# Kernel optimization log

Measured on AMD Instinct MI355X. Metric: run time of the kernel, lower is better.

Reference implementation:

```python
import jax, jax.numpy as jnp
import numpy as np

N, E, G, B, L = 24576, 98304, 512, 512, 1000
F_IN, H1, C1, C2, HID = 5, 2, 64, 128, 256


def setup_inputs() -> dict:
    key = jax.random.key(0)
    ks = jax.random.split(key, 20)
    rn = lambda k, s: jax.random.normal(k, s, jnp.float32) * 0.1
    return {
        "x": jax.random.normal(ks[0], (N, F_IN), jnp.float32),
        "edge_index": jax.random.randint(ks[1], (2, E), 0, N),
        "batch": jnp.sort(jax.random.randint(ks[2], (N,), 0, G)),
        "protein_seq": jax.random.randint(ks[3], (B, L), 0, 22),
        "W1": rn(ks[4], (F_IN, H1 * C1)), "att_src1": rn(ks[5], (H1, C1)), "att_dst1": rn(ks[6], (H1, C1)), "b1": jnp.zeros((H1 * C1,), jnp.float32),
        "W2": rn(ks[7], (H1 * C1, C2)), "att_src2": rn(ks[8], (1, C2)), "att_dst2": rn(ks[9], (1, C2)), "b2": jnp.zeros((C2,), jnp.float32),
        "Wd": rn(ks[10], (C2, HID)), "bd": jnp.zeros((HID,), jnp.float32),
        "Pe": rn(ks[11], (22, 64)),
        "K1": rn(ks[12], (64, 64, 3)), "bk1": jnp.zeros((64,), jnp.float32),
        "K2": rn(ks[13], (128, 64, 5)), "bk2": jnp.zeros((128,), jnp.float32),
        "Wp": rn(ks[14], (128, HID)), "bp": jnp.zeros((HID,), jnp.float32),
        "Wf1": rn(ks[15], (2 * HID, 128)), "bf1": jnp.zeros((128,), jnp.float32),
        "Wf2": rn(ks[16], (128, 64)), "bf2": jnp.zeros((64,), jnp.float32),
        "Wo": rn(ks[17], (64, 1)), "bo": jnp.zeros((1,), jnp.float32),
    }


def _gat(x, edge_index, W, att_src, att_dst, b, heads, out_ch):
    """PyG GATConv: add self-loops, per-edge LeakyReLU(0.2) scores, segment softmax over dst."""
    n = x.shape[0]
    h = (x @ W).reshape(n, heads, out_ch)
    loop = jnp.arange(n)
    src = jnp.concatenate([edge_index[0], loop])
    dst = jnp.concatenate([edge_index[1], loop])
    a_s = jnp.sum(h * att_src[None], axis=-1)  # [n, H]
    a_d = jnp.sum(h * att_dst[None], axis=-1)
    e = jax.nn.leaky_relu(a_s[src] + a_d[dst], negative_slope=0.2)  # [E+n, H]
    m = jax.ops.segment_max(e, dst, num_segments=n)
    w = jnp.exp(e - m[dst])
    den = jax.ops.segment_sum(w, dst, num_segments=n)
    alpha = w / (den[dst] + 1e-16)
    out = jax.ops.segment_sum(h[src] * alpha[..., None], dst, num_segments=n)
    return out.reshape(n, heads * out_ch) + b


def _conv1d(x, k, pad):  # x: [B,C,L], k: [O,I,K]
    return jax.lax.conv_general_dilated(x, k, (1,), [(pad, pad)], dimension_numbers=("NCH", "OIH", "NCH"))


def reference(x, edge_index, batch, protein_seq, W1, att_src1, att_dst1, b1, W2, att_src2, att_dst2, b2, Wd, bd, Pe, K1, bk1, K2, bk2, Wp, bp, Wf1, bf1, Wf2, bf2, Wo, bo):
    # drug branch (GAT x2 + global mean pool)
    g = jax.nn.elu(_gat(x, edge_index, W1, att_src1, att_dst1, b1, H1, C1))
    g = jax.nn.elu(_gat(g, edge_index, W2, att_src2, att_dst2, b2, 1, C2))
    sums = jax.ops.segment_sum(g, batch, num_segments=G)
    cnt = jax.ops.segment_sum(jnp.ones((g.shape[0], 1), g.dtype), batch, num_segments=G)
    drug = jax.nn.relu(sums / jnp.maximum(cnt, 1.0) @ Wd + bd)
    # protein branch (embed -> conv1d x2 -> global max pool)
    pe = Pe[protein_seq].transpose(0, 2, 1)  # [B, 64, L]
    p = jax.nn.elu(_conv1d(pe, K1, 1) + bk1[None, :, None])
    p = jax.nn.elu(_conv1d(p, K2, 2) + bk2[None, :, None])
    prot = jax.nn.relu(jnp.max(p, axis=2) @ Wp + bp)
    # head
    h = jnp.concatenate([drug, prot], axis=1)
    h = jax.nn.relu(h @ Wf1 + bf1)
    h = jax.nn.relu(h @ Wf2 + bf2)
    return h @ Wo + bo
```

## Files before the change

kernel.cpp:

```cpp
#include <hip/hip_runtime.h>
#include <hip/hip_bf16.h>
#include <math.h>

#define NN 24576
#define NE 98304
#define ETOT (NE + NN)
#define NG 512
#define NB 512
#define LL 1000
#define TL 124
#define NTILE 9

typedef __attribute__((ext_vector_type(8))) short short8;
typedef __attribute__((ext_vector_type(4))) short short4v;
typedef __attribute__((ext_vector_type(4))) float f32x4;

__device__ inline short f2bf(float x) {
    union { __hip_bfloat16 b; short s; } u;
    u.b = __float2bfloat16(x);
    return u.s;
}

__device__ inline float bf2f(short s) {
    return __uint_as_float(((unsigned)(unsigned short)s) << 16);
}

__device__ inline void atomicMaxFloat(float* addr, float val) {
    int* ai = (int*)addr;
    int old = __float_as_int(*addr);
    while (__int_as_float(old) < val) {
        int assumed = old;
        old = atomicCAS(ai, assumed, __float_as_int(val));
        if (old == assumed) break;
    }
}

__global__ void k_init(int* deg, int* cursor, float* sums, float* cnt, float* pmax) {
    int i = blockIdx.x * 256 + threadIdx.x;
    if (i < NN) { deg[i] = 0; cursor[i] = 0; }
    if (i < NG * 128) sums[i] = 0.f;
    if (i < NG) cnt[i] = 0.f;
    if (i < NB * 128) pmax[i] = -1e30f;
}

__global__ void k_count(const int* ei, int* deg) {
    int e = blockIdx.x * 256 + threadIdx.x;
    if (e >= ETOT) return;
    int d = (e < NE) ? ei[NE + e] : e - NE;
    atomicAdd(&deg[d], 1);
}

__global__ void k_scan1(const int* deg, int* excl, int* part) {
    __shared__ int s[256];
    int b = blockIdx.x, t = threadIdx.x, i = b * 256 + t;
    int v = deg[i];
    s[t] = v;
    __syncthreads();
    for (int o = 1; o < 256; o <<= 1) {
        int x = (t >= o) ? s[t - o] : 0;
        __syncthreads();
        s[t] += x;
        __syncthreads();
    }
    excl[i] = s[t] - v;
    if (t == 255) part[b] = s[t];
}

__global__ void k_scan2(int* part) {
    __shared__ int s[96];
    int t = threadIdx.x;
    if (t < 96) s[t] = part[t];
    __syncthreads();
    if (t == 0) {
        int run = 0;
        for (int i = 0; i < 96; i++) { int v = s[i]; s[i] = run; run += v; }
    }
    __syncthreads();
    if (t < 96) part[t] = s[t];
}

__global__ void k_scan3(const int* excl, const int* part, int* rowptr) {
    int i = blockIdx.x * 256 + threadIdx.x;
    rowptr[i] = excl[i] + part[i >> 8];
    if (i == 0) rowptr[NN] = ETOT;
}

__global__ void k_scatter(const int* ei, const int* rowptr, int* cursor, int* colidx) {
    int e = blockIdx.x * 256 + threadIdx.x;
    if (e >= ETOT) return;
    int s, d;
    if (e < NE) { s = ei[e]; d = ei[NE + e]; }
    else { s = d = e - NE; }
    int pos = atomicAdd(&cursor[d], 1);
    colidx[rowptr[d] + pos] = s;
}

__global__ void k_as1(const float* x, const float* wvec, float* as_, float* ad_) {
    int idx = blockIdx.x * 256 + threadIdx.x;
    if (idx >= NN * 2) return;
    int n = idx >> 1, hd = idx & 1;
    float s = 0.f, dv = 0.f;
#pragma unroll
    for (int f = 0; f < 5; f++) {
        float xv = x[n * 5 + f];
        s += xv * wvec[hd * 5 + f];
        dv += xv * wvec[10 + hd * 5 + f];
    }
    as_[idx] = s;
    ad_[idx] = dv;
}

__global__ void k_agg2x(const int* rowptr, const int* colidx, const float* x,
                        const float* as_, const float* ad_,
                        const float* W1, const float* b1, const float* wvec,
                        unsigned int* g1b, float* as2, float* ad2) {
    __shared__ float sW[640];
    __shared__ float sb1[128];
    __shared__ float swa[256];
    int t = threadIdx.x;
    for (int i = t; i < 640; i += 256) sW[i] = W1[i];
    if (t < 128) { sb1[t] = b1[t]; swa[t] = wvec[32 + t]; swa[128 + t] = wvec[160 + t]; }
    __syncthreads();

    int d = blockIdx.x * 16 + (t >> 4);
    int g = t & 15;
    int hd = (g < 5) ? 0 : 1;
    int f = (g < 5) ? g : g - 5;
    float adv = ad_[d * 2 + hd];
    int p0 = rowptr[d], p1 = rowptr[d + 1];
    float m = -1e30f, den = 0.f, acc = 0.f;
    if (g < 10) {
        for (int pc = p0; pc < p1; pc += 4) {
            int sarr[4]; float ev[4], xv[4];
#pragma unroll
            for (int i = 0; i < 4; i++) {
                int pp = pc + i;
                sarr[i] = colidx[pp < p1 ? pp : p1 - 1];
            }
#pragma unroll
            for (int i = 0; i < 4; i++) {
                ev[i] = as_[sarr[i] * 2 + hd];
                xv[i] = x[sarr[i] * 5 + f];
            }
#pragma unroll
            for (int i = 0; i < 4; i++) {
                if (pc + i < p1) {
                    float e = ev[i] + adv;
                    e = e >= 0.f ? e : 0.2f * e;
                    float nm = fmaxf(m, e);
                    float sc = __expf(m - nm);
                    float w = __expf(e - nm);
                    den = den * sc + w;
                    acc = acc * sc + w * xv[i];
                    m = nm;
                }
            }
        }
    }
    float xn = acc / (den + 1e-16f);
    int gb = (t & 63) & ~15;
    int hcol = g >> 3;
    float xs[5];
#pragma unroll
    for (int f2 = 0; f2 < 5; f2++)
        xs[f2] = __shfl(xn, gb + hcol * 5 + f2, 64);
    float ps = 0.f, pd = 0.f;
    float g1v[8];
#pragma unroll
    for (int k = 0; k < 8; k++) {
        int col = g * 8 + k;
        float v = sb1[col];
#pragma unroll
        for (int f2 = 0; f2 < 5; f2++) v += xs[f2] * sW[f2 * 128 + col];
        v = v > 0.f ? v : __expf(v) - 1.f;
        g1v[k] = v;
        ps += v * swa[col];
        pd += v * swa[128 + col];
    }
    uint4 pk;
    pk.x = ((unsigned)(unsigned short)f2bf(g1v[1]) << 16) | (unsigned)(unsigned short)f2bf(g1v[0]);
    pk.y = ((unsigned)(unsigned short)f2bf(g1v[3]) << 16) | (unsigned)(unsigned short)f2bf(g1v[2]);
    pk.z = ((unsigned)(unsigned short)f2bf(g1v[5]) << 16) | (unsigned)(unsigned short)f2bf(g1v[4]);
    pk.w = ((unsigned)(unsigned short)f2bf(g1v[7]) << 16) | (unsigned)(unsigned short)f2bf(g1v[6]);
    *(uint4*)&g1b[d * 64 + g * 4] = pk;
#pragma unroll
    for (int msk = 1; msk < 16; msk <<= 1) {
        ps += __shfl_xor(ps, msk, 64);
        pd += __shfl_xor(pd, msk, 64);
    }
    if (g == 0) { as2[d] = ps; ad2[d] = pd; }
}

__global__ void k_agg1y(const int* rowptr, const int* colidx, const unsigned int* hb,
                        const float* as_, const float* ad_, float* yacc) {
    int t = threadIdx.x;
    int d = blockIdx.x * 4 + (t >> 6);
    int c = t & 63;
    float adv = ad_[d];
    int p0 = rowptr[d], p1 = rowptr[d + 1];
    float m = -1e30f, den = 0.f, acc0 = 0.f, acc1 = 0.f;
    for (int pc = p0; pc < p1; pc += 4) {
        int sarr[4]; float ev[4]; unsigned int hv[4];
#pragma unroll
        for (int i = 0; i < 4; i++) {
            int pp = pc + i;
            sarr[i] = colidx[pp < p1 ? pp : p1 - 1];
        }
#pragma unroll
        for (int i = 0; i < 4; i++) {
            ev[i] = as_[sarr[i]];
            hv[i] = hb[sarr[i] * 64 + c];
        }
#pragma unroll
        for (int i = 0; i < 4; i++) {
            if (pc + i < p1) {
                float e = ev[i] + adv;
                e = e >= 0.f ? e : 0.2f * e;
                float nm = fmaxf(m, e);
                float sc = __expf(m - nm);
                float w = __expf(e - nm);
                den = den * sc + w;
                float h0 = __uint_as_float(hv[i] << 16);
                float h1v = __uint_as_float(hv[i] & 0xFFFF0000u);
                acc0 = acc0 * sc + w * h0;
                acc1 = acc1 * sc + w * h1v;
                m = nm;
            }
        }
    }
    float inv = 1.f / (den + 1e-16f);
    ((float2*)yacc)[d * 64 + c] = (float2){acc0 * inv, acc1 * inv};
}

#define ASTR 136
__global__ __launch_bounds__(256, 2) void k_g2mm(
    const float* yacc, const short* Bh, const short* Bl, const float* b2, float* g2) {
    __shared__ __align__(16) short Ah[64 * ASTR];
    __shared__ __align__(16) short Al[64 * ASTR];
    int t = threadIdx.x;
    int m0 = blockIdx.x * 64;
    int wv = t >> 6, lane = t & 63;
    int ln15 = lane & 15, quad = lane >> 4;

    for (int i = t; i < 64 * 32; i += 256) {
        int row = i >> 5, c4 = (i & 31) * 4;
        float4 v = *(const float4*)&yacc[(m0 + row) * 128 + c4];
        short4v hi, lo;
        hi.x = f2bf(v.x); lo.x = f2bf(v.x - bf2f(hi.x));
        hi.y = f2bf(v.y); lo.y = f2bf(v.y - bf2f(hi.y));
        hi.z = f2bf(v.z); lo.z = f2bf(v.z - bf2f(hi.z));
        hi.w = f2bf(v.w); lo.w = f2bf(v.w - bf2f(hi.w));
        *(short4v*)&Ah[row * ASTR + c4] = hi;
        *(short4v*)&Al[row * ASTR + c4] = lo;
    }
    __syncthreads();

    f32x4 acc[8];
#pragma unroll
    for (int nt = 0; nt < 8; nt++) acc[nt] = (f32x4){0.f, 0.f, 0.f, 0.f};
    int arow = wv * 16 + ln15;
#pragma unroll
    for (int kb = 0; kb < 4; kb++) {
        int koff = kb * 32 + quad * 8;
        short8 a_hi = *(const short8*)&Ah[arow * ASTR + koff];
        short8 a_lo = *(const short8*)&Al[arow * ASTR + koff];
#pragma unroll
        for (int nt = 0; nt < 8; nt++) {
            short8 bh = *(const short8*)&Bh[((kb * 8 + nt) * 64 + lane) * 8];
            short8 bl = *(const short8*)&Bl[((kb * 8 + nt) * 64 + lane) * 8];
            acc[nt] = __builtin_amdgcn_mfma_f32_16x16x32_bf16(a_hi, bh, acc[nt], 0, 0, 0);
            acc[nt] = __builtin_amdgcn_mfma_f32_16x16x32_bf16(a_hi, bl, acc[nt], 0, 0, 0);
            acc[nt] = __builtin_amdgcn_mfma_f32_16x16x32_bf16(a_lo, bh, acc[nt], 0, 0, 0);
        }
    }
#pragma unroll
    for (int nt = 0; nt < 8; nt++) {
        int col = nt * 16 + ln15;
        float bias = b2[col];
#pragma unroll
        for (int r = 0; r < 4; r++) {
            float v = acc[nt][r] + bias;
            v = v > 0.f ? v : __expf(v) - 1.f;
            int n = m0 + wv * 16 + quad * 4 + r;
            g2[n * 128 + col] = v;
        }
    }
}

__global__ void k_pool(const float* g2, const int* batch, float* sums, float* cnt) {
    __shared__ int sb[96];
    int blk = blockIdx.x, j = threadIdx.x;
    int n0 = blk * 96;
    if (j < 96) sb[j] = batch[n0 + j];
    __syncthreads();
    float v[4];
#pragma unroll
    for (int i = 0; i < 4; i++) v[i] = g2[(n0 + i) * 128 + j];
    int cur = sb[0], runStart = 0;
    float acc = 0.f;
    for (int q0 = 0; q0 < 96; q0 += 4) {
        float nv[4] = {0.f, 0.f, 0.f, 0.f};
        if (q0 + 4 < 96) {
#pragma unroll
            for (int i = 0; i < 4; i++) nv[i] = g2[(n0 + q0 + 4 + i) * 128 + j];
        }
#pragma unroll
        for (int i = 0; i < 4; i++) {
            int q = q0 + i;
            int bb = sb[q];
            if (bb != cur) {
                atomicAdd(&sums[cur * 128 + j], acc);
                if (j == 0) atomicAdd(&cnt[cur], (float)(q - runStart));
                cur = bb; acc = 0.f; runStart = q;
            }
            acc += v[i];
        }
#pragma unroll
        for (int i = 0; i < 4; i++) v[i] = nv[i];
    }
    atomicAdd(&sums[cur * 128 + j], acc);
    if (j == 0) atomicAdd(&cnt[cur], (float)(96 - runStart));
}

__global__ void k_drug_fc(const float* sums, const float* cnt, const float* Wd, const float* bd,
                          float* drug) {
    int idx = blockIdx.x * 256 + threadIdx.x;
    if (idx >= NG * 256) return;
    int g = idx >> 8, o = idx & 255;
    float c = cnt[g]; c = c < 1.f ? 1.f : c;
    float inv = 1.f / c;
    float acc = bd[o];
#pragma unroll 8
    for (int i = 0; i < 128; i++) acc += sums[g * 128 + i] * inv * Wd[i * 256 + o];
    drug[idx] = acc > 0.f ? acc : 0.f;
}

__global__ void k_prep_w(const float* K1, const float* K2, const float* W2, const float* Pe,
                         const float* W1, const float* as1c, const float* ad1c,
                         const float* as2c, const float* ad2c,
                         short* Bswz1, short* Bswz2, short* Bh2, short* Bl2, short* Peb,
                         float* wvec) {
    int idx = blockIdx.x * 256 + threadIdx.x;
    if (idx < 22 * 64) Peb[idx] = f2bf(Pe[idx]);
    if (idx < 20) {
        int q = idx % 10, hd = q / 5, f = q % 5;
        const float* av = (idx < 10) ? as1c : ad1c;
        float s = 0.f;
        for (int c = 0; c < 64; c++) s += W1[f * 128 + hd * 64 + c] * av[hd * 64 + c];
        wvec[idx < 10 ? q : 10 + q] = s;
    }
    if (idx >= 32 && idx < 288) {
        int q = idx - 32;
        int kk = q & 127;
        const float* av = (q < 128) ? as2c : ad2c;
        float s = 0.f;
        for (int n2 = 0; n2 < 128; n2++) s += W2[kk * 128 + n2] * av[n2];
        wvec[idx] = s;
    }
    if (idx < 192 * 64) {
        int j = idx & 7, lane = (idx >> 3) & 63, rest = idx >> 9;
        int nt = rest & 3, kb = rest >> 2;
        int k = kb * 32 + ((lane >> 4) << 3) + j;
        int n = nt * 16 + (lane & 15);
        int kk = k >> 6, i = k & 63;
        Bswz1[idx] = f2bf(K1[n * 192 + i * 3 + kk]);
    }
    if (idx < 320 * 128) {
        int j = idx & 7, lane = (idx >> 3) & 63, rest = idx >> 9;
        int nt = rest & 7, kb = rest >> 3;
        int k = kb * 32 + ((lane >> 4) << 3) + j;
        int n = nt * 16 + (lane & 15);
        int kk = k / 64, i = k % 64;
        Bswz2[idx] = f2bf(K2[n * 320 + i * 5 + kk]);
    }
    if (idx < 128 * 128) {
        int j = idx & 7, lane = (idx >> 3) & 63, rest = idx >> 9;
        int nt = rest & 7, kb = rest >> 3;
        int k = kb * 32 + ((lane >> 4) << 3) + j;
        int n = nt * 16 + (lane & 15);
        float v = W2[k * 128 + n];
        short hh = f2bf(v);
        Bh2[idx] = hh;
        Bl2[idx] = f2bf(v - bf2f(hh));
    }
}

#define SSTR 72
__global__ __launch_bounds__(256, 4) void k_protein(
    const int* seq, const short* Peb, const short* Bswz1, const float* bk1,
    const short* Bswz2, const float* bk2, float* pmax) {
    __shared__ __align__(16) short sEmb[130 * SSTR];
    __shared__ __align__(16) short s1[132 * SSTR];

    int b = blockIdx.x / NTILE;
    int tile = blockIdx.x - b * NTILE;
    int t0 = tile * TL;
    int t = threadIdx.x;
    int wv = t >> 6, lane = t & 63;
    int ln15 = lane & 15, quad = lane >> 4;
    int mhalf = wv & 1, nhalf = wv >> 1;

    for (int j0 = 0; j0 < 130; j0 += 64) {
        int j = j0 + (t >> 2);
        if (j < 130) {
            int c0 = (t & 3) * 16;
            int l = t0 - 3 + j;
            int id = (l >= 0 && l < LL) ? seq[b * LL + l] : -1;
            short* dst = &sEmb[j * SSTR + c0];
            if (id >= 0) {
                const short8* src = (const short8*)&Peb[id * 64 + c0];
                *(short8*)dst = src[0];
                *(short8*)(dst + 8) = src[1];
            } else {
                *(short8*)dst = (short8){0, 0, 0, 0, 0, 0, 0, 0};
                *(short8*)(dst + 8) = (short8){0, 0, 0, 0, 0, 0, 0, 0};
            }
        }
    }
    s1[(128 + (t >> 6)) * SSTR + (t & 63)] = 0;
    __syncthreads();

    {
        f32x4 acc[4][2];
#pragma unroll
        for (int mi = 0; mi < 4; mi++)
#pragma unroll
            for (int ni = 0; ni < 2; ni++) acc[mi][ni] = (f32x4){0.f, 0.f, 0.f, 0.f};
#pragma unroll
        for (int kb = 0; kb < 6; kb++) {
            int koff = kb * 32 + quad * 8;
            int kk = koff >> 6, i0 = koff & 63;
            short8 b0 = *(const short8*)&Bswz1[((kb * 4 + nhalf * 2 + 0) * 64 + lane) * 8];
            short8 b1 = *(const short8*)&Bswz1[((kb * 4 + nhalf * 2 + 1) * 64 + lane) * 8];
#pragma unroll
            for (int mi = 0; mi < 4; mi++) {
                int arow = (mhalf * 4 + mi) * 16 + ln15 + kk;
                short8 a = *(const short8*)&sEmb[arow * SSTR + i0];
                acc[mi][0] = __builtin_amdgcn_mfma_f32_16x16x32_bf16(a, b0, acc[mi][0], 0, 0, 0);
                acc[mi][1] = __builtin_amdgcn_mfma_f32_16x16x32_bf16(a, b1, acc[mi][1], 0, 0, 0);
            }
        }
#pragma unroll
        for (int mi = 0; mi < 4; mi++) {
            int mt = mhalf * 4 + mi;
#pragma unroll
            for (int ni = 0; ni < 2; ni++) {
                int col = (nhalf * 2 + ni) * 16 + ln15;
                float bias = bk1[col];
#pragma unroll
                for (int r = 0; r < 4; r++) {
                    int q = mt * 16 + quad * 4 + r;
                    int l = t0 - 2 + q;
                    float v = acc[mi][ni][r] + bias;
                    v = v > 0.f ? v : __expf(v) - 1.f;
                    s1[q * SSTR + col] = (l >= 0 && l < LL) ? f2bf(v) : (short)0;
                }
            }
        }
    }
    __syncthreads();

    f32x4 acc2[4][4];
#pragma unroll
    for (int mi = 0; mi < 4; mi++)
#pragma unroll
        for (int ni = 0; ni < 4; ni++) acc2[mi][ni] = (f32x4){0.f, 0.f, 0.f, 0.f};
#pragma unroll 2
    for (int kb = 0; kb < 10; kb++) {
        int koff = kb * 32 + quad * 8;
        int kk = koff >> 6, i0 = koff & 63;
        short8 a[4], bb[4];
#pragma unroll
        for (int mi = 0; mi < 4; mi++) {
            int arow = (mhalf * 4 + mi) * 16 + ln15 + kk;
            a[mi] = *(const short8*)&s1[arow * SSTR + i0];
        }
#pragma unroll
        for (int ni = 0; ni < 4; ni++)
            bb[ni] = *(const short8*)&Bswz2[((kb * 8 + nhalf * 4 + ni) * 64 + lane) * 8];
#pragma unroll
        for (int mi = 0; mi < 4; mi++)
#pragma unroll
            for (int ni = 0; ni < 4; ni++)
                acc2[mi][ni] = __builtin_amdgcn_mfma_f32_16x16x32_bf16(a[mi], bb[ni], acc2[mi][ni], 0, 0, 0);
    }

#pragma unroll
    for (int ni = 0; ni < 4; ni++) {
        int col = (nhalf * 4 + ni) * 16 + ln15;
        float mx = -1e30f;
#pragma unroll
        for (int mi = 0; mi < 4; mi++) {
#pragma unroll
            for (int r = 0; r < 4; r++) {
                int p = (mhalf * 4 + mi) * 16 + quad * 4 + r;
                if (p < TL && t0 + p < LL) mx = fmaxf(mx, acc2[mi][ni][r]);
            }
        }
        mx = fmaxf(mx, __shfl_xor(mx, 16, 64));
        mx = fmaxf(mx, __shfl_xor(mx, 32, 64));
        if (quad == 0) {
            float v = mx + bk2[col];
            v = v > 0.f ? v : __expf(v) - 1.f;
            atomicMaxFloat(&pmax[b * 128 + col], v);
        }
    }
}

__global__ void k_prot_fc(const float* pmax, const float* Wp, const float* bp, float* prot) {
    int idx = blockIdx.x * 256 + threadIdx.x;
    if (idx >= NB * 256) return;
    int g = idx >> 8, o = idx & 255;
    float acc = bp[o];
#pragma unroll 8
    for (int i = 0; i < 128; i++) acc += pmax[g * 128 + i] * Wp[i * 256 + o];
    prot[idx] = acc > 0.f ? acc : 0.f;
}

__global__ void k_head(const float* drug, const float* prot, const float* Wf1, const float* bf1,
                       const float* Wf2, const float* bf2, const float* Wo, const float* bo,
                       float* out) {
    __shared__ float in[512];
    __shared__ float hh[128];
    __shared__ float h2s[64];
    int g = blockIdx.x, t = threadIdx.x;
    in[t] = drug[g * 256 + t];
    in[128 + t] = drug[g * 256 + 128 + t];
    in[256 + t] = prot[g * 256 + t];
    in[384 + t] = prot[g * 256 + 128 + t];
    __syncthreads();
    float acc = bf1[t];
#pragma unroll 8
    for (int c = 0; c < 512; c++) acc += in[c] * Wf1[c * 128 + t];
    hh[t] = acc > 0.f ? acc : 0.f;
    __syncthreads();
    if (t < 64) {
        float a2 = bf2[t];
#pragma unroll 8
        for (int c = 0; c < 128; c++) a2 += hh[c] * Wf2[c * 64 + t];
        h2s[t] = a2 > 0.f ? a2 : 0.f;
    }
    __syncthreads();
    if (t == 0) {
        float o = bo[0];
#pragma unroll 8
        for (int c = 0; c < 64; c++) o += h2s[c] * Wo[c];
        out[g] = o;
    }
}

extern "C" void kernel_launch(void* const* d_in, const int* in_sizes, int n_in,
                              void* d_out, int out_size, void* d_ws, size_t ws_size,
                              hipStream_t stream) {
    (void)in_sizes; (void)n_in; (void)out_size; (void)ws_size;
    const float* x   = (const float*)d_in[0];
    const int* ei    = (const int*)d_in[1];
    const int* batch = (const int*)d_in[2];
    const int* seq   = (const int*)d_in[3];
    const float* W1  = (const float*)d_in[4];
    const float* a_s1 = (const float*)d_in[5];
    const float* a_d1 = (const float*)d_in[6];
    const float* b1  = (const float*)d_in[7];
    const float* W2  = (const float*)d_in[8];
    const float* a_s2 = (const float*)d_in[9];
    const float* a_d2 = (const float*)d_in[10];
    const float* b2  = (const float*)d_in[11];
    const float* Wd  = (const float*)d_in[12];
    const float* bd  = (const float*)d_in[13];
    const float* Pe  = (const float*)d_in[14];
    const float* K1  = (const float*)d_in[15];
    const float* bk1 = (const float*)d_in[16];
    const float* K2  = (const float*)d_in[17];
    const float* bk2 = (const float*)d_in[18];
    const float* Wp  = (const float*)d_in[19];
    const float* bp  = (const float*)d_in[20];
    const float* Wf1 = (const float*)d_in[21];
    const float* bf1 = (const float*)d_in[22];
    const float* Wf2 = (const float*)d_in[23];
    const float* bf2 = (const float*)d_in[24];
    const float* Wo  = (const float*)d_in[25];
    const float* bo  = (const float*)d_in[26];
    float* out = (float*)d_out;

    float* w = (float*)d_ws;
    float* g1bf = w; w += NN * 64;
    float* yacc = w; w += NN * 128;
    float* g2   = w; w += NN * 128;
    float* as1  = w; w += NN * 2;
    float* ad1  = w; w += NN * 2;
    float* as2  = w; w += NN;
    float* ad2  = w; w += NN;
    float* sums = w; w += NG * 128;
    float* cnt  = w; w += NG;
    float* drug = w; w += NG * 256;
    float* prot = w; w += NB * 256;
    float* pmax = w; w += NB * 128;
    float* wvec = w; w += 512;
    short* Bswz1 = (short*)w; w += 192 * 64 / 2;
    short* Bswz2 = (short*)w; w += 320 * 128 / 2;
    short* Bh2  = (short*)w; w += 128 * 128 / 2;
    short* Bl2  = (short*)w; w += 128 * 128 / 2;
    short* Peb  = (short*)w; w += 22 * 64 / 2 + 8;
    int* deg    = (int*)w; w += NN;
    int* cursor = (int*)w; w += NN;
    int* excl   = (int*)w; w += NN;
    int* part   = (int*)w; w += 128;
    int* rowptr = (int*)w; w += NN + 8;
    int* colidx = (int*)w; w += ETOT;

    unsigned int* g1b = (unsigned int*)g1bf;

    hipLaunchKernelGGL(k_init, dim3(256), dim3(256), 0, stream, deg, cursor, sums, cnt, pmax);
    hipLaunchKernelGGL(k_prep_w, dim3(160), dim3(256), 0, stream,
                       K1, K2, W2, Pe, W1, a_s1, a_d1, a_s2, a_d2,
                       Bswz1, Bswz2, Bh2, Bl2, Peb, wvec);

    hipLaunchKernelGGL(k_count, dim3(ETOT / 256), dim3(256), 0, stream, ei, deg);
    hipLaunchKernelGGL(k_scan1, dim3(NN / 256), dim3(256), 0, stream, deg, excl, part);
    hipLaunchKernelGGL(k_scan2, dim3(1), dim3(128), 0, stream, part);
    hipLaunchKernelGGL(k_scan3, dim3(NN / 256), dim3(256), 0, stream, excl, part, rowptr);
    hipLaunchKernelGGL(k_scatter, dim3(ETOT / 256), dim3(256), 0, stream, ei, rowptr, cursor, colidx);

    hipLaunchKernelGGL(k_protein, dim3(NB * NTILE), dim3(256), 0, stream,
                       seq, Peb, Bswz1, bk1, Bswz2, bk2, pmax);
    hipLaunchKernelGGL(k_prot_fc, dim3(NB), dim3(256), 0, stream, pmax, Wp, bp, prot);

    hipLaunchKernelGGL(k_as1, dim3(NN * 2 / 256), dim3(256), 0, stream, x, wvec, as1, ad1);
    hipLaunchKernelGGL(k_agg2x, dim3(NN / 16), dim3(256), 0, stream,
                       rowptr, colidx, x, as1, ad1, W1, b1, wvec, g1b, as2, ad2);

    hipLaunchKernelGGL(k_agg1y, dim3(NN / 4), dim3(256), 0, stream,
                       rowptr, colidx, g1b, as2, ad2, yacc);
    hipLaunchKernelGGL(k_g2mm, dim3(NN / 64), dim3(256), 0, stream,
                       yacc, Bh2, Bl2, b2, g2);

    hipLaunchKernelGGL(k_pool, dim3(NN / 96), dim3(128), 0, stream, g2, batch, sums, cnt);
    hipLaunchKernelGGL(k_drug_fc, dim3(NG), dim3(256), 0, stream, sums, cnt, Wd, bd, drug);

    hipLaunchKernelGGL(k_head, dim3(NG), dim3(128), 0, stream,
                       drug, prot, Wf1, bf1, Wf2, bf2, Wo, bo, out);
}
```

Measured before the change: 322.2 us.

## Merge small kernels to cut launches and overlap edge counting with protein conv

Folds init and weight prep into one launch, and runs degree counting and first-layer attention scores as extra blocks of the protein conv kernel so they overlap with it. Scan stages 2 and 3 are merged, with each block recomputing its own prefix. The protein FC, drug FC and MLP head become a single tail kernel, which removes the intermediate drug and prot buffers. The aim is to cut launch overhead and idle gaps between small kernels. In exchange, the protein kernel's grid is mixed with lightweight blocks that share its launch bounds and LDS allocation.

```diff
diff --git a/kernel.cpp b/kernel.cpp
--- a/kernel.cpp
+++ b/kernel.cpp
@@ -10,6 +10,9 @@
 #define LL 1000
 #define TL 124
 #define NTILE 9
+#define PROT_BLKS (NB * NTILE)
+#define CNT_BLKS (ETOT / 256)
+#define AS1_BLKS (NN * 2 / 256)
 
 typedef __attribute__((ext_vector_type(8))) short short8;
 typedef __attribute__((ext_vector_type(4))) short short4v;
@@ -35,312 +38,22 @@
     }
 }
 
-__global__ void k_init(int* deg, int* cursor, float* sums, float* cnt, float* pmax) {
-    int i = blockIdx.x * 256 + threadIdx.x;
-    if (i < NN) { deg[i] = 0; cursor[i] = 0; }
-    if (i < NG * 128) sums[i] = 0.f;
-    if (i < NG) cnt[i] = 0.f;
-    if (i < NB * 128) pmax[i] = -1e30f;
-}
-
-__global__ void k_count(const int* ei, int* deg) {
-    int e = blockIdx.x * 256 + threadIdx.x;
-    if (e >= ETOT) return;
-    int d = (e < NE) ? ei[NE + e] : e - NE;
-    atomicAdd(&deg[d], 1);
-}
-
-__global__ void k_scan1(const int* deg, int* excl, int* part) {
-    __shared__ int s[256];
-    int b = blockIdx.x, t = threadIdx.x, i = b * 256 + t;
-    int v = deg[i];
-    s[t] = v;
-    __syncthreads();
-    for (int o = 1; o < 256; o <<= 1) {
-        int x = (t >= o) ? s[t - o] : 0;
-        __syncthreads();
-        s[t] += x;
-        __syncthreads();
-    }
-    excl[i] = s[t] - v;
-    if (t == 255) part[b] = s[t];
-}
-
-__global__ void k_scan2(int* part) {
-    __shared__ int s[96];
-    int t = threadIdx.x;
-    if (t < 96) s[t] = part[t];
-    __syncthreads();
-    if (t == 0) {
-        int run = 0;
-        for (int i = 0; i < 96; i++) { int v = s[i]; s[i] = run; run += v; }
-    }
-    __syncthreads();
-    if (t < 96) part[t] = s[t];
-}
-
-__global__ void k_scan3(const int* excl, const int* part, int* rowptr) {
-    int i = blockIdx.x * 256 + threadIdx.x;
-    rowptr[i] = excl[i] + part[i >> 8];
-    if (i == 0) rowptr[NN] = ETOT;
-}
-
-__global__ void k_scatter(const int* ei, const int* rowptr, int* cursor, int* colidx) {
-    int e = blockIdx.x * 256 + threadIdx.x;
-    if (e >= ETOT) return;
-    int s, d;
-    if (e < NE) { s = ei[e]; d = ei[NE + e]; }
-    else { s = d = e - NE; }
-    int pos = atomicAdd(&cursor[d], 1);
-    colidx[rowptr[d] + pos] = s;
-}
-
-__global__ void k_as1(const float* x, const float* wvec, float* as_, float* ad_) {
-    int idx = blockIdx.x * 256 + threadIdx.x;
-    if (idx >= NN * 2) return;
-    int n = idx >> 1, hd = idx & 1;
-    float s = 0.f, dv = 0.f;
-#pragma unroll
-    for (int f = 0; f < 5; f++) {
-        float xv = x[n * 5 + f];
-        s += xv * wvec[hd * 5 + f];
-        dv += xv * wvec[10 + hd * 5 + f];
-    }
-    as_[idx] = s;
-    ad_[idx] = dv;
-}
-
-__global__ void k_agg2x(const int* rowptr, const int* colidx, const float* x,
-                        const float* as_, const float* ad_,
-                        const float* W1, const float* b1, const float* wvec,
-                        unsigned int* g1b, float* as2, float* ad2) {
-    __shared__ float sW[640];
-    __shared__ float sb1[128];
-    __shared__ float swa[256];
-    int t = threadIdx.x;
-    for (int i = t; i < 640; i += 256) sW[i] = W1[i];
-    if (t < 128) { sb1[t] = b1[t]; swa[t] = wvec[32 + t]; swa[128 + t] = wvec[160 + t]; }
-    __syncthreads();
-
-    int d = blockIdx.x * 16 + (t >> 4);
-    int g = t & 15;
-    int hd = (g < 5) ? 0 : 1;
-    int f = (g < 5) ? g : g - 5;
-    float adv = ad_[d * 2 + hd];
-    int p0 = rowptr[d], p1 = rowptr[d + 1];
-    float m = -1e30f, den = 0.f, acc = 0.f;
-    if (g < 10) {
-        for (int pc = p0; pc < p1; pc += 4) {
-            int sarr[4]; float ev[4], xv[4];
-#pragma unroll
-            for (int i = 0; i < 4; i++) {
-                int pp = pc + i;
-                sarr[i] = colidx[pp < p1 ? pp : p1 - 1];
-            }
-#pragma unroll
-            for (int i = 0; i < 4; i++) {
-                ev[i] = as_[sarr[i] * 2 + hd];
-                xv[i] = x[sarr[i] * 5 + f];
-            }
-#pragma unroll
-            for (int i = 0; i < 4; i++) {
-                if (pc + i < p1) {
-                    float e = ev[i] + adv;
-                    e = e >= 0.f ? e : 0.2f * e;
-                    float nm = fmaxf(m, e);
-                    float sc = __expf(m - nm);
-                    float w = __expf(e - nm);
-                    den = den * sc + w;
-                    acc = acc * sc + w * xv[i];
-                    m = nm;
-                }
-            }
-        }
-    }
-    float xn = acc / (den + 1e-16f);
-    int gb = (t & 63) & ~15;
-    int hcol = g >> 3;
-    float xs[5];
-#pragma unroll
-    for (int f2 = 0; f2 < 5; f2++)
-        xs[f2] = __shfl(xn, gb + hcol * 5 + f2, 64);
-    float ps = 0.f, pd = 0.f;
-    float g1v[8];
-#pragma unroll
-    for (int k = 0; k < 8; k++) {
-        int col = g * 8 + k;
-        float v = sb1[col];
-#pragma unroll
-        for (int f2 = 0; f2 < 5; f2++) v += xs[f2] * sW[f2 * 128 + col];
-        v = v > 0.f ? v : __expf(v) - 1.f;
-        g1v[k] = v;
-        ps += v * swa[col];
-        pd += v * swa[128 + col];
-    }
-    uint4 pk;
-    pk.x = ((unsigned)(unsigned short)f2bf(g1v[1]) << 16) | (unsigned)(unsigned short)f2bf(g1v[0]);
-    pk.y = ((unsigned)(unsigned short)f2bf(g1v[3]) << 16) | (unsigned)(unsigned short)f2bf(g1v[2]);
-    pk.z = ((unsigned)(unsigned short)f2bf(g1v[5]) << 16) | (unsigned)(unsigned short)f2bf(g1v[4]);
-    pk.w = ((unsigned)(unsigned short)f2bf(g1v[7]) << 16) | (unsigned)(unsigned short)f2bf(g1v[6]);
-    *(uint4*)&g1b[d * 64 + g * 4] = pk;
-#pragma unroll
-    for (int msk = 1; msk < 16; msk <<= 1) {
-        ps += __shfl_xor(ps, msk, 64);
-        pd += __shfl_xor(pd, msk, 64);
-    }
-    if (g == 0) { as2[d] = ps; ad2[d] = pd; }
-}
-
-__global__ void k_agg1y(const int* rowptr, const int* colidx, const unsigned int* hb,
-                        const float* as_, const float* ad_, float* yacc) {
-    int t = threadIdx.x;
-    int d = blockIdx.x * 4 + (t >> 6);
-    int c = t & 63;
-    float adv = ad_[d];
-    int p0 = rowptr[d], p1 = rowptr[d + 1];
-    float m = -1e30f, den = 0.f, acc0 = 0.f, acc1 = 0.f;
-    for (int pc = p0; pc < p1; pc += 4) {
-        int sarr[4]; float ev[4]; unsigned int hv[4];
-#pragma unroll
-        for (int i = 0; i < 4; i++) {
-            int pp = pc + i;
-            sarr[i] = colidx[pp < p1 ? pp : p1 - 1];
-        }
-#pragma unroll
-        for (int i = 0; i < 4; i++) {
-            ev[i] = as_[sarr[i]];
-            hv[i] = hb[sarr[i] * 64 + c];
-        }
-#pragma unroll
-        for (int i = 0; i < 4; i++) {
-            if (pc + i < p1) {
-                float e = ev[i] + adv;
-                e = e >= 0.f ? e : 0.2f * e;
-                float nm = fmaxf(m, e);
-                float sc = __expf(m - nm);
-                float w = __expf(e - nm);
-                den = den * sc + w;
-                float h0 = __uint_as_float(hv[i] << 16);
-                float h1v = __uint_as_float(hv[i] & 0xFFFF0000u);
-                acc0 = acc0 * sc + w * h0;
-                acc1 = acc1 * sc + w * h1v;
-                m = nm;
-            }
-        }
-    }
-    float inv = 1.f / (den + 1e-16f);
-    ((float2*)yacc)[d * 64 + c] = (float2){acc0 * inv, acc1 * inv};
-}
-
-#define ASTR 136
-__global__ __launch_bounds__(256, 2) void k_g2mm(
-    const float* yacc, const short* Bh, const short* Bl, const float* b2, float* g2) {
-    __shared__ __align__(16) short Ah[64 * ASTR];
-    __shared__ __align__(16) short Al[64 * ASTR];
-    int t = threadIdx.x;
-    int m0 = blockIdx.x * 64;
-    int wv = t >> 6, lane = t & 63;
-    int ln15 = lane & 15, quad = lane >> 4;
-
-    for (int i = t; i < 64 * 32; i += 256) {
-        int row = i >> 5, c4 = (i & 31) * 4;
-        float4 v = *(const float4*)&yacc[(m0 + row) * 128 + c4];
-        short4v hi, lo;
-        hi.x = f2bf(v.x); lo.x = f2bf(v.x - bf2f(hi.x));
-        hi.y = f2bf(v.y); lo.y = f2bf(v.y - bf2f(hi.y));
-        hi.z = f2bf(v.z); lo.z = f2bf(v.z - bf2f(hi.z));
-        hi.w = f2bf(v.w); lo.w = f2bf(v.w - bf2f(hi.w));
-        *(short4v*)&Ah[row * ASTR + c4] = hi;
-        *(short4v*)&Al[row * ASTR + c4] = lo;
-    }
-    __syncthreads();
-
-    f32x4 acc[8];
-#pragma unroll
-    for (int nt = 0; nt < 8; nt++) acc[nt] = (f32x4){0.f, 0.f, 0.f, 0.f};
-    int arow = wv * 16 + ln15;
-#pragma unroll
-    for (int kb = 0; kb < 4; kb++) {
-        int koff = kb * 32 + quad * 8;
-        short8 a_hi = *(const short8*)&Ah[arow * ASTR + koff];
-        short8 a_lo = *(const short8*)&Al[arow * ASTR + koff];
-#pragma unroll
-        for (int nt = 0; nt < 8; nt++) {
-            short8 bh = *(const short8*)&Bh[((kb * 8 + nt) * 64 + lane) * 8];
-            short8 bl = *(const short8*)&Bl[((kb * 8 + nt) * 64 + lane) * 8];
-            acc[nt] = __builtin_amdgcn_mfma_f32_16x16x32_bf16(a_hi, bh, acc[nt], 0, 0, 0);
-            acc[nt] = __builtin_amdgcn_mfma_f32_16x16x32_bf16(a_hi, bl, acc[nt], 0, 0, 0);
-            acc[nt] = __builtin_amdgcn_mfma_f32_16x16x32_bf16(a_lo, bh, acc[nt], 0, 0, 0);
-        }
-    }
-#pragma unroll
-    for (int nt = 0; nt < 8; nt++) {
-        int col = nt * 16 + ln15;
-        float bias = b2[col];
-#pragma unroll
-        for (int r = 0; r < 4; r++) {
-            float v = acc[nt][r] + bias;
-            v = v > 0.f ? v : __expf(v) - 1.f;
-            int n = m0 + wv * 16 + quad * 4 + r;
-            g2[n * 128 + col] = v;
-        }
-    }
-}
-
-__global__ void k_pool(const float* g2, const int* batch, float* sums, float* cnt) {
-    __shared__ int sb[96];
-    int blk = blockIdx.x, j = threadIdx.x;
-    int n0 = blk * 96;
-    if (j < 96) sb[j] = batch[n0 + j];
-    __syncthreads();
-    float v[4];
-#pragma unroll
-    for (int i = 0; i < 4; i++) v[i] = g2[(n0 + i) * 128 + j];
-    int cur = sb[0], runStart = 0;
-    float acc = 0.f;
-    for (int q0 = 0; q0 < 96; q0 += 4) {
-        float nv[4] = {0.f, 0.f, 0.f, 0.f};
-        if (q0 + 4 < 96) {
-#pragma unroll
-            for (int i = 0; i < 4; i++) nv[i] = g2[(n0 + q0 + 4 + i) * 128 + j];
-        }
-#pragma unroll
-        for (int i = 0; i < 4; i++) {
-            int q = q0 + i;
-            int bb = sb[q];
-            if (bb != cur) {
-                atomicAdd(&sums[cur * 128 + j], acc);
-                if (j == 0) atomicAdd(&cnt[cur], (float)(q - runStart));
-                cur = bb; acc = 0.f; runStart = q;
-            }
-            acc += v[i];
-        }
-#pragma unroll
-        for (int i = 0; i < 4; i++) v[i] = nv[i];
-    }
-    atomicAdd(&sums[cur * 128 + j], acc);
-    if (j == 0) atomicAdd(&cnt[cur], (float)(96 - runStart));
-}
-
-__global__ void k_drug_fc(const float* sums, const float* cnt, const float* Wd, const float* bd,
-                          float* drug) {
-    int idx = blockIdx.x * 256 + threadIdx.x;
-    if (idx >= NG * 256) return;
-    int g = idx >> 8, o = idx & 255;
-    float c = cnt[g]; c = c < 1.f ? 1.f : c;
-    float inv = 1.f / c;
-    float acc = bd[o];
-#pragma unroll 8
-    for (int i = 0; i < 128; i++) acc += sums[g * 128 + i] * inv * Wd[i * 256 + o];
-    drug[idx] = acc > 0.f ? acc : 0.f;
-}
-
-__global__ void k_prep_w(const float* K1, const float* K2, const float* W2, const float* Pe,
-                         const float* W1, const float* as1c, const float* ad1c,
-                         const float* as2c, const float* ad2c,
-                         short* Bswz1, short* Bswz2, short* Bh2, short* Bl2, short* Peb,
-                         float* wvec) {
-    int idx = blockIdx.x * 256 + threadIdx.x;
+__global__ void k_init_prep(int* deg, int* cursor, float* sums, float* cnt, float* pmax,
+                            const float* K1, const float* K2, const float* W2, const float* Pe,
+                            const float* W1, const float* as1c, const float* ad1c,
+                            const float* as2c, const float* ad2c,
+                            short* Bswz1, short* Bswz2, short* Bh2, short* Bl2, short* Peb,
+                            float* wvec) {
+    int bid = blockIdx.x, t = threadIdx.x;
+    if (bid < 256) {
+        int i = bid * 256 + t;
+        if (i < NN) { deg[i] = 0; cursor[i] = 0; }
+        if (i < NG * 128) sums[i] = 0.f;
+        if (i < NG) cnt[i] = 0.f;
+        if (i < NB * 128) pmax[i] = -1e30f;
+        return;
+    }
+    int idx = (bid - 256) * 256 + t;
     if (idx < 22 * 64) Peb[idx] = f2bf(Pe[idx]);
     if (idx < 20) {
         int q = idx % 10, hd = q / 5, f = q % 5;
@@ -386,16 +99,42 @@
 }
 
 #define SSTR 72
-__global__ __launch_bounds__(256, 4) void k_protein(
+__global__ __launch_bounds__(256, 4) void k_prot_cnt_as1(
     const int* seq, const short* Peb, const short* Bswz1, const float* bk1,
-    const short* Bswz2, const float* bk2, float* pmax) {
+    const short* Bswz2, const float* bk2, float* pmax,
+    const int* ei, int* deg,
+    const float* x, const float* wvec, float* as1o, float* ad1o) {
+    int bid = blockIdx.x;
+    int t = threadIdx.x;
+
+    if (bid >= PROT_BLKS) {
+        int rb = bid - PROT_BLKS;
+        if (rb < CNT_BLKS) {
+            int e = rb * 256 + t;
+            int d = (e < NE) ? ei[NE + e] : e - NE;
+            atomicAdd(&deg[d], 1);
+        } else {
+            int idx = (rb - CNT_BLKS) * 256 + t;
+            int n = idx >> 1, hd = idx & 1;
+            float s = 0.f, dv = 0.f;
+#pragma unroll
+            for (int f = 0; f < 5; f++) {
+                float xv = x[n * 5 + f];
+                s += xv * wvec[hd * 5 + f];
+                dv += xv * wvec[10 + hd * 5 + f];
+            }
+            as1o[idx] = s;
+            ad1o[idx] = dv;
+        }
+        return;
+    }
+
     __shared__ __align__(16) short sEmb[130 * SSTR];
     __shared__ __align__(16) short s1[132 * SSTR];
 
-    int b = blockIdx.x / NTILE;
-    int tile = blockIdx.x - b * NTILE;
+    int b = bid / NTILE;
+    int tile = bid - b * NTILE;
     int t0 = tile * TL;
-    int t = threadIdx.x;
     int wv = t >> 6, lane = t & 63;
     int ln15 = lane & 15, quad = lane >> 4;
     int mhalf = wv & 1, nhalf = wv >> 1;
@@ -507,44 +246,301 @@
     }
 }
 
-__global__ void k_prot_fc(const float* pmax, const float* Wp, const float* bp, float* prot) {
-    int idx = blockIdx.x * 256 + threadIdx.x;
-    if (idx >= NB * 256) return;
-    int g = idx >> 8, o = idx & 255;
-    float acc = bp[o];
-#pragma unroll 8
-    for (int i = 0; i < 128; i++) acc += pmax[g * 128 + i] * Wp[i * 256 + o];
-    prot[idx] = acc > 0.f ? acc : 0.f;
-}
-
-__global__ void k_head(const float* drug, const float* prot, const float* Wf1, const float* bf1,
-                       const float* Wf2, const float* bf2, const float* Wo, const float* bo,
-                       float* out) {
-    __shared__ float in[512];
+__global__ void k_scan1(const int* deg, int* excl, int* part) {
+    __shared__ int s[256];
+    int b = blockIdx.x, t = threadIdx.x, i = b * 256 + t;
+    int v = deg[i];
+    s[t] = v;
+    __syncthreads();
+    for (int o = 1; o < 256; o <<= 1) {
+        int x = (t >= o) ? s[t - o] : 0;
+        __syncthreads();
+        s[t] += x;
+        __syncthreads();
+    }
+    excl[i] = s[t] - v;
+    if (t == 255) part[b] = s[t];
+}
+
+__global__ void k_scan23(const int* excl, const int* part, int* rowptr) {
+    __shared__ int sp[96];
+    __shared__ int pref;
+    int b = blockIdx.x, t = threadIdx.x;
+    if (t < 96) sp[t] = part[t];
+    __syncthreads();
+    if (t == 0) {
+        int run = 0;
+        for (int i = 0; i < b; i++) run += sp[i];
+        pref = run;
+    }
+    __syncthreads();
+    int i = b * 256 + t;
+    rowptr[i] = excl[i] + pref;
+    if (i == 0) rowptr[NN] = ETOT;
+}
+
+__global__ void k_scatter(const int* ei, const int* rowptr, int* cursor, int* colidx) {
+    int e = blockIdx.x * 256 + threadIdx.x;
+    if (e >= ETOT) return;
+    int s, d;
+    if (e < NE) { s = ei[e]; d = ei[NE + e]; }
+    else { s = d = e - NE; }
+    int pos = atomicAdd(&cursor[d], 1);
+    colidx[rowptr[d] + pos] = s;
+}
+
+__global__ void k_agg2x(const int* rowptr, const int* colidx, const float* x,
+                        const float* as_, const float* ad_,
+                        const float* W1, const float* b1, const float* wvec,
+                        unsigned int* g1b, float* as2, float* ad2) {
+    __shared__ float sW[640];
+    __shared__ float sb1[128];
+    __shared__ float swa[256];
+    int t = threadIdx.x;
+    for (int i = t; i < 640; i += 256) sW[i] = W1[i];
+    if (t < 128) { sb1[t] = b1[t]; swa[t] = wvec[32 + t]; swa[128 + t] = wvec[160 + t]; }
+    __syncthreads();
+
+    int d = blockIdx.x * 16 + (t >> 4);
+    int g = t & 15;
+    int hd = (g < 5) ? 0 : 1;
+    int f = (g < 5) ? g : g - 5;
+    float adv = ad_[d * 2 + hd];
+    int p0 = rowptr[d], p1 = rowptr[d + 1];
+    float m = -1e30f, den = 0.f, acc = 0.f;
+    if (g < 10) {
+        for (int pc = p0; pc < p1; pc += 4) {
+            int sarr[4]; float ev[4], xv[4];
+#pragma unroll
+            for (int i = 0; i < 4; i++) {
+                int pp = pc + i;
+                sarr[i] = colidx[pp < p1 ? pp : p1 - 1];
+            }
+#pragma unroll
+            for (int i = 0; i < 4; i++) {
+                ev[i] = as_[sarr[i] * 2 + hd];
+                xv[i] = x[sarr[i] * 5 + f];
+            }
+#pragma unroll
+            for (int i = 0; i < 4; i++) {
+                if (pc + i < p1) {
+                    float e = ev[i] + adv;
+                    e = e >= 0.f ? e : 0.2f * e;
+                    float nm = fmaxf(m, e);
+                    float sc = __expf(m - nm);
+                    float w = __expf(e - nm);
+                    den = den * sc + w;
+                    acc = acc * sc + w * xv[i];
+                    m = nm;
+                }
+            }
+        }
+    }
+    float xn = acc / (den + 1e-16f);
+    int gb = (t & 63) & ~15;
+    int hcol = g >> 3;
+    float xs[5];
+#pragma unroll
+    for (int f2 = 0; f2 < 5; f2++)
+        xs[f2] = __shfl(xn, gb + hcol * 5 + f2, 64);
+    float ps = 0.f, pd = 0.f;
+    float g1v[8];
+#pragma unroll
+    for (int k = 0; k < 8; k++) {
+        int col = g * 8 + k;
+        float v = sb1[col];
+#pragma unroll
+        for (int f2 = 0; f2 < 5; f2++) v += xs[f2] * sW[f2 * 128 + col];
+        v = v > 0.f ? v : __expf(v) - 1.f;
+        g1v[k] = v;
+        ps += v * swa[col];
+        pd += v * swa[128 + col];
+    }
+    uint4 pk;
+    pk.x = ((unsigned)(unsigned short)f2bf(g1v[1]) << 16) | (unsigned)(unsigned short)f2bf(g1v[0]);
+    pk.y = ((unsigned)(unsigned short)f2bf(g1v[3]) << 16) | (unsigned)(unsigned short)f2bf(g1v[2]);
+    pk.z = ((unsigned)(unsigned short)f2bf(g1v[5]) << 16) | (unsigned)(unsigned short)f2bf(g1v[4]);
+    pk.w = ((unsigned)(unsigned short)f2bf(g1v[7]) << 16) | (unsigned)(unsigned short)f2bf(g1v[6]);
+    *(uint4*)&g1b[d * 64 + g * 4] = pk;
+#pragma unroll
+    for (int msk = 1; msk < 16; msk <<= 1) {
+        ps += __shfl_xor(ps, msk, 64);
+        pd += __shfl_xor(pd, msk, 64);
+    }
+    if (g == 0) { as2[d] = ps; ad2[d] = pd; }
+}
+
+__global__ void k_agg1y(const int* rowptr, const int* colidx, const unsigned int* hb,
+                        const float* as_, const float* ad_, float* yacc) {
+    int t = threadIdx.x;
+    int d = blockIdx.x * 4 + (t >> 6);
+    int c = t & 63;
+    float adv = ad_[d];
+    int p0 = rowptr[d], p1 = rowptr[d + 1];
+    float m = -1e30f, den = 0.f, acc0 = 0.f, acc1 = 0.f;
+    for (int pc = p0; pc < p1; pc += 4) {
+        int sarr[4]; float ev[4]; unsigned int hv[4];
+#pragma unroll
+        for (int i = 0; i < 4; i++) {
+            int pp = pc + i;
+            sarr[i] = colidx[pp < p1 ? pp : p1 - 1];
+        }
+#pragma unroll
+        for (int i = 0; i < 4; i++) {
+            ev[i] = as_[sarr[i]];
+            hv[i] = hb[sarr[i] * 64 + c];
+        }
+#pragma unroll
+        for (int i = 0; i < 4; i++) {
+            if (pc + i < p1) {
+                float e = ev[i] + adv;
+                e = e >= 0.f ? e : 0.2f * e;
+                float nm = fmaxf(m, e);
+                float sc = __expf(m - nm);
+                float w = __expf(e - nm);
+                den = den * sc + w;
+                float h0 = __uint_as_float(hv[i] << 16);
+                float h1v = __uint_as_float(hv[i] & 0xFFFF0000u);
+                acc0 = acc0 * sc + w * h0;
+                acc1 = acc1 * sc + w * h1v;
+                m = nm;
+            }
+        }
+    }
+    float inv = 1.f / (den + 1e-16f);
+    ((float2*)yacc)[d * 64 + c] = (float2){acc0 * inv, acc1 * inv};
+}
+
+#define ASTR 136
+__global__ __launch_bounds__(256, 2) void k_g2mm(
+    const float* yacc, const short* Bh, const short* Bl, const float* b2, float* g2) {
+    __shared__ __align__(16) short Ah[64 * ASTR];
+    __shared__ __align__(16) short Al[64 * ASTR];
+    int t = threadIdx.x;
+    int m0 = blockIdx.x * 64;
+    int wv = t >> 6, lane = t & 63;
+    int ln15 = lane & 15, quad = lane >> 4;
+
+    for (int i = t; i < 64 * 32; i += 256) {
+        int row = i >> 5, c4 = (i & 31) * 4;
+        float4 v = *(const float4*)&yacc[(m0 + row) * 128 + c4];
+        short4v hi, lo;
+        hi.x = f2bf(v.x); lo.x = f2bf(v.x - bf2f(hi.x));
+        hi.y = f2bf(v.y); lo.y = f2bf(v.y - bf2f(hi.y));
+        hi.z = f2bf(v.z); lo.z = f2bf(v.z - bf2f(hi.z));
+        hi.w = f2bf(v.w); lo.w = f2bf(v.w - bf2f(hi.w));
+        *(short4v*)&Ah[row * ASTR + c4] = hi;
+        *(short4v*)&Al[row * ASTR + c4] = lo;
+    }
+    __syncthreads();
+
+    f32x4 acc[8];
+#pragma unroll
+    for (int nt = 0; nt < 8; nt++) acc[nt] = (f32x4){0.f, 0.f, 0.f, 0.f};
+    int arow = wv * 16 + ln15;
+#pragma unroll
+    for (int kb = 0; kb < 4; kb++) {
+        int koff = kb * 32 + quad * 8;
+        short8 a_hi = *(const short8*)&Ah[arow * ASTR + koff];
+        short8 a_lo = *(const short8*)&Al[arow * ASTR + koff];
+#pragma unroll
+        for (int nt = 0; nt < 8; nt++) {
+            short8 bh = *(const short8*)&Bh[((kb * 8 + nt) * 64 + lane) * 8];
+            short8 bl = *(const short8*)&Bl[((kb * 8 + nt) * 64 + lane) * 8];
+            acc[nt] = __builtin_amdgcn_mfma_f32_16x16x32_bf16(a_hi, bh, acc[nt], 0, 0, 0);
+            acc[nt] = __builtin_amdgcn_mfma_f32_16x16x32_bf16(a_hi, bl, acc[nt], 0, 0, 0);
+            acc[nt] = __builtin_amdgcn_mfma_f32_16x16x32_bf16(a_lo, bh, acc[nt], 0, 0, 0);
+        }
+    }
+#pragma unroll
+    for (int nt = 0; nt < 8; nt++) {
+        int col = nt * 16 + ln15;
+        float bias = b2[col];
+#pragma unroll
+        for (int r = 0; r < 4; r++) {
+            float v = acc[nt][r] + bias;
+            v = v > 0.f ? v : __expf(v) - 1.f;
+            int n = m0 + wv * 16 + quad * 4 + r;
+            g2[n * 128 + col] = v;
+        }
+    }
+}
+
+__global__ void k_pool(const float* g2, const int* batch, float* sums, float* cnt) {
+    __shared__ int sb[96];
+    int blk = blockIdx.x, j = threadIdx.x;
+    int n0 = blk * 96;
+    if (j < 96) sb[j] = batch[n0 + j];
+    __syncthreads();
+    float v[4];
+#pragma unroll
+    for (int i = 0; i < 4; i++) v[i] = g2[(n0 + i) * 128 + j];
+    int cur = sb[0], runStart = 0;
+    float acc = 0.f;
+    for (int q0 = 0; q0 < 96; q0 += 4) {
+        float nv[4] = {0.f, 0.f, 0.f, 0.f};
+        if (q0 + 4 < 96) {
+#pragma unroll
+            for (int i = 0; i < 4; i++) nv[i] = g2[(n0 + q0 + 4 + i) * 128 + j];
+        }
+#pragma unroll
+        for (int i = 0; i < 4; i++) {
+            int q = q0 + i;
+            int bb = sb[q];
+            if (bb != cur) {
+                atomicAdd(&sums[cur * 128 + j], acc);
+                if (j == 0) atomicAdd(&cnt[cur], (float)(q - runStart));
+                cur = bb; acc = 0.f; runStart = q;
+            }
+            acc += v[i];
+        }
+#pragma unroll
+        for (int i = 0; i < 4; i++) v[i] = nv[i];
+    }
+    atomicAdd(&sums[cur * 128 + j], acc);
+    if (j == 0) atomicAdd(&cnt[cur], (float)(96 - runStart));
+}
+
+__global__ void k_tail(const float* pmax, const float* Wp, const float* bp,
+                       const float* sums, const float* cnt, const float* Wd, const float* bd,
+                       const float* Wf1, const float* bf1, const float* Wf2, const float* bf2,
+                       const float* Wo, const float* bo, float* out) {
+    __shared__ float in2[512];
     __shared__ float hh[128];
     __shared__ float h2s[64];
     int g = blockIdx.x, t = threadIdx.x;
-    in[t] = drug[g * 256 + t];
-    in[128 + t] = drug[g * 256 + 128 + t];
-    in[256 + t] = prot[g * 256 + t];
-    in[384 + t] = prot[g * 256 + 128 + t];
-    __syncthreads();
-    float acc = bf1[t];
+
+    float pacc = bp[t];
 #pragma unroll 8
-    for (int c = 0; c < 512; c++) acc += in[c] * Wf1[c * 128 + t];
-    hh[t] = acc > 0.f ? acc : 0.f;
+    for (int i = 0; i < 128; i++) pacc += pmax[g * 128 + i] * Wp[i * 256 + t];
+    in2[256 + t] = pacc > 0.f ? pacc : 0.f;
+
+    float c = cnt[g]; c = c < 1.f ? 1.f : c;
+    float inv = 1.f / c;
+    float dacc = bd[t];
+#pragma unroll 8
+    for (int i = 0; i < 128; i++) dacc += sums[g * 128 + i] * inv * Wd[i * 256 + t];
+    in2[t] = dacc > 0.f ? dacc : 0.f;
+    __syncthreads();
+
+    if (t < 128) {
+        float acc = bf1[t];
+#pragma unroll 8
+        for (int cc = 0; cc < 512; cc++) acc += in2[cc] * Wf1[cc * 128 + t];
+        hh[t] = acc > 0.f ? acc : 0.f;
+    }
     __syncthreads();
     if (t < 64) {
         float a2 = bf2[t];
 #pragma unroll 8
-        for (int c = 0; c < 128; c++) a2 += hh[c] * Wf2[c * 64 + t];
+        for (int cc = 0; cc < 128; cc++) a2 += hh[cc] * Wf2[cc * 64 + t];
         h2s[t] = a2 > 0.f ? a2 : 0.f;
     }
     __syncthreads();
     if (t == 0) {
         float o = bo[0];
 #pragma unroll 8
-        for (int c = 0; c < 64; c++) o += h2s[c] * Wo[c];
+        for (int cc = 0; cc < 64; cc++) o += h2s[cc] * Wo[cc];
         out[g] = o;
     }
 }
@@ -592,8 +588,6 @@
     float* ad2  = w; w += NN;
     float* sums = w; w += NG * 128;
     float* cnt  = w; w += NG;
-    float* drug = w; w += NG * 256;
-    float* prot = w; w += NB * 256;
     float* pmax = w; w += NB * 128;
     float* wvec = w; w += 512;
     short* Bswz1 = (short*)w; w += 192 * 64 / 2;
@@ -610,33 +604,30 @@
 
     unsigned int* g1b = (unsigned int*)g1bf;
 
-    hipLaunchKernelGGL(k_init, dim3(256), dim3(256), 0, stream, deg, cursor, sums, cnt, pmax);
-    hipLaunchKernelGGL(k_prep_w, dim3(160), dim3(256), 0, stream,
+    hipLaunchKernelGGL(k_init_prep, dim3(256 + 160), dim3(256), 0, stream,
+                       deg, cursor, sums, cnt, pmax,
                        K1, K2, W2, Pe, W1, a_s1, a_d1, a_s2, a_d2,
                        Bswz1, Bswz2, Bh2, Bl2, Peb, wvec);
 
-    hipLaunchKernelGGL(k_count, dim3(ETOT / 256), dim3(256), 0, stream, ei, deg);
+    hipLaunchKernelGGL(k_prot_cnt_as1, dim3(PROT_BLKS + CNT_BLKS + AS1_BLKS), dim3(256), 0, stream,
+                       seq, Peb, Bswz1, bk1, Bswz2, bk2, pmax,
+                       ei, deg, x, wvec, as1, ad1);
+
     hipLaunchKernelGGL(k_scan1, dim3(NN / 256), dim3(256), 0, stream, deg, excl, part);
-    hipLaunchKernelGGL(k_scan2, dim3(1), dim3(128), 0, stream, part);
-    hipLaunchKernelGGL(k_scan3, dim3(NN / 256), dim3(256), 0, stream, excl, part, rowptr);
+    hipLaunchKernelGGL(k_scan23, dim3(NN / 256), dim3(256), 0, stream, excl, part, rowptr);
     hipLaunchKernelGGL(k_scatter, dim3(ETOT / 256), dim3(256), 0, stream, ei, rowptr, cursor, colidx);
 
-    hipLaunchKernelGGL(k_protein, dim3(NB * NTILE), dim3(256), 0, stream,
-                       seq, Peb, Bswz1, bk1, Bswz2, bk2, pmax);
-    hipLaunchKernelGGL(k_prot_fc, dim3(NB), dim3(256), 0, stream, pmax, Wp, bp, prot);
-
-    hipLaunchKernelGGL(k_as1, dim3(NN * 2 / 256), dim3(256), 0, stream, x, wvec, as1, ad1);
     hipLaunchKernelGGL(k_agg2x, dim3(NN / 16), dim3(256), 0, stream,
                        rowptr, colidx, x, as1, ad1, W1, b1, wvec, g1b, as2, ad2);
 
     hipLaunchKernelGGL(k_agg1y, dim3(NN / 4), dim3(256), 0, stream,
                        rowptr, colidx, g1b, as2, ad2, yacc);
+
     hipLaunchKernelGGL(k_g2mm, dim3(NN / 64), dim3(256), 0, stream,
                        yacc, Bh2, Bl2, b2, g2);
 
     hipLaunchKernelGGL(k_pool, dim3(NN / 96), dim3(128), 0, stream, g2, batch, sums, cnt);
-    hipLaunchKernelGGL(k_drug_fc, dim3(NG), dim3(256), 0, stream, sums, cnt, Wd, bd, drug);
-
-    hipLaunchKernelGGL(k_head, dim3(NG), dim3(128), 0, stream,
-                       drug, prot, Wf1, bf1, Wf2, bf2, Wo, bo, out);
-}
+
+    hipLaunchKernelGGL(k_tail, dim3(NG), dim3(256), 0, stream,
+                       pmax, Wp, bp, sums, cnt, Wd, bd, Wf1, bf1, Wf2, bf2, Wo, bo, out);
+}
```

After: 305.5 us. -5.2%, faster.
